# Kernel tuning notes

Hardware: AMD Instinct MI355X
Metric: run time of the kernel (lower is better)

Reference implementation:

```python
import jax, jax.numpy as jnp
import numpy as np

L = 9  # local window size


def local_windows(x, l):
    # x: (n, c, h, w) -> (n, c, l*l, h, w): all l*l shifted views (zero-padded),
    # equivalent to F.unfold(x, kernel=(l,l), stride=1, padding=l//2).
    n, c, h, w = x.shape
    pad = l // 2
    xp = jnp.pad(x, ((0, 0), (0, 0), (pad, pad), (pad, pad)))
    views = [xp[:, :, i:i + h, j:j + w] for i in range(l) for j in range(l)]
    return jnp.stack(views, axis=2)


def setup_inputs() -> dict:
    key = jax.random.key(0)
    k1, k2, k3 = jax.random.split(key, 3)
    n, c, h, w = 2, 128, 64, 64
    ft = jax.random.normal(k1, (n, c, h, w), dtype=jnp.float32)
    fk = jax.random.normal(k2, (n, c, h, w), dtype=jnp.float32)
    # 1x1 conv weight shared between key and query projections: (out_c, in_c)
    W = jax.random.normal(k3, (128, 128), dtype=jnp.float32) * (1.0 / np.sqrt(128))
    return {"ft": ft, "fk": fk, "W": W}


def reference(ft, fk, W):
    # 1x1 conv == channel matmul
    key = jnp.einsum('oi,nihw->nohw', W, ft)    # key from frame t
    query = jnp.einsum('oi,nihw->nohw', W, fk)  # query from frame k
    # f_similar(query, key, L): per-pixel query dotted with L*L local keys
    key_win = local_windows(key, L)             # (n, c, L*L, h, w)
    sim = jnp.einsum('nchw,nckhw->nhwk', query, key_win)  # (n, h, w, L*L)
    weight = jax.nn.softmax(sim, axis=-1)
    # f_weighting(ft, weight, L): weighted sum of L*L local raw-ft vectors
    ft_win = local_windows(ft, L)                # (n, c, L*L, h, w)
    out = jnp.einsum('nckhw,nhwk->nchw', ft_win, weight)
    return out
```

## Files before the change

### kernel.cpp

```cpp
#include <hip/hip_runtime.h>
#include <hip/hip_bf16.h>


#define Hh 64
#define Ww 64
#define Cc 128
#define Nn 2
#define KK 81
#define HW (Hh * Ww)
#define CHW (Cc * HW)
#define P_TOT (Nn * HW)

typedef _Float16 h8 __attribute__((ext_vector_type(8)));
typedef _Float16 h4 __attribute__((ext_vector_type(4)));
typedef _Float16 h2 __attribute__((ext_vector_type(2)));
typedef float f4v __attribute__((ext_vector_type(4)));

__device__ __forceinline__ float dot8(const h8 a, const h8 b, float acc) {
#if __has_builtin(__builtin_amdgcn_fdot2)
    h2 a0 = {a[0], a[1]}, b0 = {b[0], b[1]};
    h2 a1 = {a[2], a[3]}, b1 = {b[2], b[3]};
    h2 a2 = {a[4], a[5]}, b2 = {b[4], b[5]};
    h2 a3 = {a[6], a[7]}, b3 = {b[6], b[7]};
    acc = __builtin_amdgcn_fdot2(a0, b0, acc, false);
    acc = __builtin_amdgcn_fdot2(a1, b1, acc, false);
    acc = __builtin_amdgcn_fdot2(a2, b2, acc, false);
    acc = __builtin_amdgcn_fdot2(a3, b3, acc, false);
#else
#pragma unroll
    for (int i = 0; i < 8; ++i) acc += (float)a[i] * (float)b[i];
#endif
    return acc;
}

__global__ __launch_bounds__(256) void proj_kernel(const float* __restrict__ ft,
                                                   const float* __restrict__ fk,
                                                   const float* __restrict__ Wm,
                                                   _Float16* __restrict__ Qbuf,
                                                   _Float16* __restrict__ Kbuf,
                                                   _Float16* __restrict__ fth) {
    __shared__ __align__(16) _Float16 Wth[128 * 136];
    __shared__ __align__(16) _Float16 xkh[32 * 136];
    __shared__ __align__(16) _Float16 xqh[32 * 136];
    const int t = threadIdx.x;
    const int p0 = blockIdx.x * 32;
    const int nn = p0 >> 12;
    const int gbase = nn * CHW + (p0 & 4095);

#pragma unroll 4
    for (int e = t; e < 4096; e += 256) {
        const int n = e >> 5, ch = e & 31;
        const float4 v = *(const float4*)&Wm[n * 128 + (ch << 2)];
        h4 hv; hv[0] = (_Float16)v.x; hv[1] = (_Float16)v.y;
               hv[2] = (_Float16)v.z; hv[3] = (_Float16)v.w;
        *(h4*)&Wth[n * 136 + (ch << 2)] = hv;
    }
#pragma unroll 4
    for (int e = t; e < 1024; e += 256) {
        const int c = e >> 3, pc = e & 7;
        const float4 vk = *(const float4*)&ft[gbase + c * HW + (pc << 2)];
        const float4 vq = *(const float4*)&fk[gbase + c * HW + (pc << 2)];
        const int px = pc << 2;
        xkh[(px    ) * 136 + c] = (_Float16)vk.x;
        xkh[(px + 1) * 136 + c] = (_Float16)vk.y;
        xkh[(px + 2) * 136 + c] = (_Float16)vk.z;
        xkh[(px + 3) * 136 + c] = (_Float16)vk.w;
        xqh[(px    ) * 136 + c] = (_Float16)vq.x;
        xqh[(px + 1) * 136 + c] = (_Float16)vq.y;
        xqh[(px + 2) * 136 + c] = (_Float16)vq.z;
        xqh[(px + 3) * 136 + c] = (_Float16)vq.w;
    }
    __syncthreads();

#pragma unroll
    for (int e = t; e < 512; e += 256) {
        const int px = e >> 4, cq = e & 15;
        *(h8*)&fth[(size_t)(p0 + px) * 128 + (cq << 3)] =
            *(const h8*)&xkh[px * 136 + (cq << 3)];
    }

    const int lane = t & 63, wv = t >> 6;
    const int quad = lane >> 4, l15 = lane & 15;
    const _Float16* xs = (wv >> 1) ? xqh : xkh;
    _Float16* dst = (wv >> 1) ? Qbuf : Kbuf;
    const int mt = wv & 1;
    const int abase = (mt * 16 + l15) * 136 + (quad << 3);
    const h8 a0 = *(const h8*)&xs[abase];
    const h8 a1 = *(const h8*)&xs[abase + 32];
    const h8 a2 = *(const h8*)&xs[abase + 64];
    const h8 a3 = *(const h8*)&xs[abase + 96];
#pragma unroll
    for (int nt = 0; nt < 8; ++nt) {
        const int bbase = (nt * 16 + l15) * 136 + (quad << 3);
        const h8 b0 = *(const h8*)&Wth[bbase];
        const h8 b1 = *(const h8*)&Wth[bbase + 32];
        const h8 b2 = *(const h8*)&Wth[bbase + 64];
        const h8 b3 = *(const h8*)&Wth[bbase + 96];
        f4v acc = {0.f, 0.f, 0.f, 0.f};
        acc = __builtin_amdgcn_mfma_f32_16x16x32_f16(a0, b0, acc, 0, 0, 0);
        acc = __builtin_amdgcn_mfma_f32_16x16x32_f16(a1, b1, acc, 0, 0, 0);
        acc = __builtin_amdgcn_mfma_f32_16x16x32_f16(a2, b2, acc, 0, 0, 0);
        acc = __builtin_amdgcn_mfma_f32_16x16x32_f16(a3, b3, acc, 0, 0, 0);
        const int col = nt * 16 + l15;
        const size_t rb = (size_t)(p0 + mt * 16 + (quad << 2)) * 128 + col;
#pragma unroll
        for (int r = 0; r < 4; ++r)
            dst[rb + (size_t)r * 128] = (_Float16)acc[r];
    }
}

__global__ __launch_bounds__(256, 4) void sim_weight_kernel(const _Float16* __restrict__ Qbuf,
                                                            const _Float16* __restrict__ Kbuf,
                                                            const _Float16* __restrict__ fth,
                                                            float* __restrict__ out) {
    __shared__ __align__(16) unsigned char smem[40720];
    _Float16* Ksw  = (_Float16*)smem;
    _Float16* Qsw  = (_Float16*)(smem + 36864);
    _Float16* ftl  = (_Float16*)smem;
    _Float16* simb = (_Float16*)(smem + 39168);
    float*    redM = (float*)(smem + 40464);
    float*    redS = (float*)(smem + 40592);

    const int t  = threadIdx.x;
    const int b  = blockIdx.x;
    const int x0 = (b & 7) << 3;
    const int y  = (b >> 3) & 63;
    const int nn = b >> 9;
    const int pg0 = (nn << 12) + (y << 6) + x0;

#pragma unroll 3
    for (int e = t; e < 144 * 16; e += 256) {
        const int v = e >> 4, ci = e & 15;
        const int gx = x0 + (v & 15) - 4;
        const int gy = y + (v >> 4) - 4;
        h8 val = {0, 0, 0, 0, 0, 0, 0, 0};
        if ((unsigned)gx < 64u && (unsigned)gy < 64u)
            val = *(const h8*)&Kbuf[(size_t)((nn << 12) + (gy << 6) + gx) * 128 + (ci << 3)];
        *(h8*)&Ksw[(v << 7) + ((ci ^ (v & 15)) << 3)] = val;
    }
    if (t < 128) {
        const int v = t >> 4, ci = t & 15;
        *(h8*)&Qsw[(v << 7) + ((ci ^ v) << 3)] =
            *(const h8*)&Qbuf[(size_t)(pg0 + v) * 128 + (ci << 3)];
    }
    __syncthreads();

    const int p = t & 7, kb = t >> 3;
    const bool has2 = (kb + 64 < KK);
    const int k0 = kb, k1 = kb + 32, k2 = has2 ? kb + 64 : kb;
    const int v0 = (k0 / 9) * 16 + p + k0 % 9;
    const int v1 = (k1 / 9) * 16 + p + k1 % 9;
    const int v2 = (k2 / 9) * 16 + p + k2 % 9;
    const int b0 = v0 << 7, m0 = v0 & 15;
    const int b1 = v1 << 7, m1 = v1 & 15;
    const int b2 = v2 << 7, m2 = v2 & 15;
    const int bq = p << 7;
    float s0 = 0.f, s1 = 0.f, s2 = 0.f;
#pragma unroll 4
    for (int ci = 0; ci < 16; ++ci) {
        const h8 q8 = *(const h8*)&Qsw[bq + ((ci ^ p) << 3)];
        const h8 kA = *(const h8*)&Ksw[b0 + ((ci ^ m0) << 3)];
        const h8 kB = *(const h8*)&Ksw[b1 + ((ci ^ m1) << 3)];
        const h8 kC = *(const h8*)&Ksw[b2 + ((ci ^ m2) << 3)];
        s0 = dot8(q8, kA, s0);
        s1 = dot8(q8, kB, s1);
        s2 = dot8(q8, kC, s2);
    }
    __syncthreads();

#pragma unroll 3
    for (int e = t; e < 144 * 16; e += 256) {
        const int v = e >> 4, ci = e & 15;
        const int gx = x0 + (v & 15) - 4;
        const int gy = y + (v >> 4) - 4;
        h8 val = {0, 0, 0, 0, 0, 0, 0, 0};
        if ((unsigned)gx < 64u && (unsigned)gy < 64u)
            val = *(const h8*)&fth[(size_t)((nn << 12) + (gy << 6) + gx) * 128 + (ci << 3)];
        *(h8*)&ftl[v * 136 + (ci << 3)] = val;
    }

    float m = fmaxf(s0, s1);
    if (has2) m = fmaxf(m, s2);
#pragma unroll
    for (int off = 8; off <= 32; off <<= 1) m = fmaxf(m, __shfl_xor(m, off));
    if ((t & 56) == 0) redM[((t >> 6) << 3) + p] = m;
    __syncthreads();
    float mm = fmaxf(fmaxf(redM[p], redM[8 + p]), fmaxf(redM[16 + p], redM[24 + p]));
    const float e0 = __expf(s0 - mm);
    const float e1 = __expf(s1 - mm);
    const float e2 = has2 ? __expf(s2 - mm) : 0.f;
    simb[k0 * 8 + p] = (_Float16)e0;
    simb[k1 * 8 + p] = (_Float16)e1;
    if (has2) simb[(kb + 64) * 8 + p] = (_Float16)e2;
    float s = e0 + e1 + e2;
#pragma unroll
    for (int off = 8; off <= 32; off <<= 1) s += __shfl_xor(s, off);
    if ((t & 56) == 0) redS[((t >> 6) << 3) + p] = s;
    __syncthreads();
    const float inv = 1.f / (redS[p] + redS[8 + p] + redS[16 + p] + redS[24 + p]);

    const int cq = t >> 3;
    float4 acc = make_float4(0, 0, 0, 0);
    for (int r = 0; r < 9; ++r) {
        const int rb = ((r << 4) + p) * 136 + (cq << 2);
        const int k9 = r * 9;
#pragma unroll
        for (int dx = 0; dx < 9; ++dx) {
            const float w = (float)simb[(k9 + dx) * 8 + p];
            const h4 f = *(const h4*)&ftl[rb + dx * 136];
            acc.x += (float)f[0] * w;
            acc.y += (float)f[1] * w;
            acc.z += (float)f[2] * w;
            acc.w += (float)f[3] * w;
        }
    }
    const size_t ob = (size_t)((nn * Cc + (cq << 2)) << 12) + (y << 6) + x0 + p;
    out[ob]          = acc.x * inv;
    out[ob + HW]     = acc.y * inv;
    out[ob + 2*HW]   = acc.z * inv;
    out[ob + 3*HW]   = acc.w * inv;
}

extern "C" void kernel_launch(void* const* d_in, const int* in_sizes, int n_in,
                              void* d_out, int out_size, void* d_ws, size_t ws_size,
                              hipStream_t stream) {
    const float* ft = (const float*)d_in[0];
    const float* fk = (const float*)d_in[1];
    const float* Wm = (const float*)d_in[2];
    float* out = (float*)d_out;

    _Float16* wsh  = (_Float16*)d_ws;
    _Float16* Qbuf = wsh;
    _Float16* Kbuf = wsh + 1048576;
    _Float16* fth  = wsh + 2097152;

    proj_kernel<<<256, 256, 0, stream>>>(ft, fk, Wm, Qbuf, Kbuf, fth);
    sim_weight_kernel<<<1024, 256, 0, stream>>>(Qbuf, Kbuf, fth, out);
}
```

Before: 80.52 us.

## Compute local similarity scores with MFMA instead of per-thread fdot2

Replaces the scalar fdot2 dot-product loop for query-key similarity with 16x16x32 f16 MFMA tiles, one per window row. Each wave multiplies 16 key positions against the 8 queries (padded to 16) and scatters the valid diagonal band of results into shared memory, from which the softmax stage reads them. This cuts VALU work and per-thread LDS traffic. In exchange it adds two barriers and computes many unused products, since only a band of each tile is kept and half the query rows are duplicates.

```diff
diff --git a/kernel.cpp b/kernel.cpp
--- a/kernel.cpp
+++ b/kernel.cpp
@@ -13,25 +13,7 @@
 
 typedef _Float16 h8 __attribute__((ext_vector_type(8)));
 typedef _Float16 h4 __attribute__((ext_vector_type(4)));
-typedef _Float16 h2 __attribute__((ext_vector_type(2)));
 typedef float f4v __attribute__((ext_vector_type(4)));
-
-__device__ __forceinline__ float dot8(const h8 a, const h8 b, float acc) {
-#if __has_builtin(__builtin_amdgcn_fdot2)
-    h2 a0 = {a[0], a[1]}, b0 = {b[0], b[1]};
-    h2 a1 = {a[2], a[3]}, b1 = {b[2], b[3]};
-    h2 a2 = {a[4], a[5]}, b2 = {b[4], b[5]};
-    h2 a3 = {a[6], a[7]}, b3 = {b[6], b[7]};
-    acc = __builtin_amdgcn_fdot2(a0, b0, acc, false);
-    acc = __builtin_amdgcn_fdot2(a1, b1, acc, false);
-    acc = __builtin_amdgcn_fdot2(a2, b2, acc, false);
-    acc = __builtin_amdgcn_fdot2(a3, b3, acc, false);
-#else
-#pragma unroll
-    for (int i = 0; i < 8; ++i) acc += (float)a[i] * (float)b[i];
-#endif
-    return acc;
-}
 
 __global__ __launch_bounds__(256) void proj_kernel(const float* __restrict__ ft,
                                                    const float* __restrict__ fk,
@@ -117,6 +99,7 @@
     _Float16* Ksw  = (_Float16*)smem;
     _Float16* Qsw  = (_Float16*)(smem + 36864);
     _Float16* ftl  = (_Float16*)smem;
+    float*    simbF= (float*)smem;
     _Float16* simb = (_Float16*)(smem + 39168);
     float*    redM = (float*)(smem + 40464);
     float*    redS = (float*)(smem + 40592);
@@ -145,27 +128,45 @@
     }
     __syncthreads();
 
+    const int lane = t & 63, wv = t >> 6;
+    const int quad = lane >> 4, l15 = lane & 15;
+    const int qrow = l15 & 7;
+    h8 qb[4];
+#pragma unroll
+    for (int kc = 0; kc < 4; ++kc) {
+        const int ci = (kc << 2) + quad;
+        qb[kc] = *(const h8*)&Qsw[(qrow << 7) + ((ci ^ qrow) << 3)];
+    }
+    const int r0 = wv, r1 = wv + 4;
+    f4v acc0 = {0.f,0.f,0.f,0.f}, acc1 = acc0, acc2 = acc0;
+#pragma unroll
+    for (int kc = 0; kc < 4; ++kc) {
+        const int ci = (kc << 2) + quad;
+        const h8 kA = *(const h8*)&Ksw[(((r0 << 4) + l15) << 7) + ((ci ^ l15) << 3)];
+        const h8 kB = *(const h8*)&Ksw[(((r1 << 4) + l15) << 7) + ((ci ^ l15) << 3)];
+        const h8 kC = *(const h8*)&Ksw[(((8  << 4) + l15) << 7) + ((ci ^ l15) << 3)];
+        acc0 = __builtin_amdgcn_mfma_f32_16x16x32_f16(kA, qb[kc], acc0, 0, 0, 0);
+        acc1 = __builtin_amdgcn_mfma_f32_16x16x32_f16(kB, qb[kc], acc1, 0, 0, 0);
+        acc2 = __builtin_amdgcn_mfma_f32_16x16x32_f16(kC, qb[kc], acc2, 0, 0, 0);
+    }
+    __syncthreads();
+
+#pragma unroll
+    for (int reg = 0; reg < 4; ++reg) {
+        const int xx = (quad << 2) + reg;
+        const int dx = xx - l15;
+        const bool ok = (l15 < 8) && (dx >= 0) && (dx < 9);
+        if (ok)            simbF[(r0 * 9 + dx) * 8 + l15] = acc0[reg];
+        if (ok)            simbF[(r1 * 9 + dx) * 8 + l15] = acc1[reg];
+        if (ok && wv == 0) simbF[(8  * 9 + dx) * 8 + l15] = acc2[reg];
+    }
+    __syncthreads();
+
     const int p = t & 7, kb = t >> 3;
     const bool has2 = (kb + 64 < KK);
-    const int k0 = kb, k1 = kb + 32, k2 = has2 ? kb + 64 : kb;
-    const int v0 = (k0 / 9) * 16 + p + k0 % 9;
-    const int v1 = (k1 / 9) * 16 + p + k1 % 9;
-    const int v2 = (k2 / 9) * 16 + p + k2 % 9;
-    const int b0 = v0 << 7, m0 = v0 & 15;
-    const int b1 = v1 << 7, m1 = v1 & 15;
-    const int b2 = v2 << 7, m2 = v2 & 15;
-    const int bq = p << 7;
-    float s0 = 0.f, s1 = 0.f, s2 = 0.f;
-#pragma unroll 4
-    for (int ci = 0; ci < 16; ++ci) {
-        const h8 q8 = *(const h8*)&Qsw[bq + ((ci ^ p) << 3)];
-        const h8 kA = *(const h8*)&Ksw[b0 + ((ci ^ m0) << 3)];
-        const h8 kB = *(const h8*)&Ksw[b1 + ((ci ^ m1) << 3)];
-        const h8 kC = *(const h8*)&Ksw[b2 + ((ci ^ m2) << 3)];
-        s0 = dot8(q8, kA, s0);
-        s1 = dot8(q8, kB, s1);
-        s2 = dot8(q8, kC, s2);
-    }
+    const float s0 = simbF[kb * 8 + p];
+    const float s1 = simbF[(kb + 32) * 8 + p];
+    const float s2 = has2 ? simbF[(kb + 64) * 8 + p] : 0.f;
     __syncthreads();
 
 #pragma unroll 3
@@ -189,8 +190,8 @@
     const float e0 = __expf(s0 - mm);
     const float e1 = __expf(s1 - mm);
     const float e2 = has2 ? __expf(s2 - mm) : 0.f;
-    simb[k0 * 8 + p] = (_Float16)e0;
-    simb[k1 * 8 + p] = (_Float16)e1;
+    simb[kb * 8 + p] = (_Float16)e0;
+    simb[(kb + 32) * 8 + p] = (_Float16)e1;
     if (has2) simb[(kb + 64) * 8 + p] = (_Float16)e2;
     float s = e0 + e1 + e2;
 #pragma unroll
```

Measured after the change: 79.21 us. About the same (-1.6%).
